# Kernel tuning notes

Hardware: AMD Instinct MI355X
Metric: run time of the kernel (lower is better)

Reference implementation:

```python
import jax, jax.numpy as jnp
import numpy as np

N = 12500      # nodes
E = 200000     # edges (avg degree 16)
IN = 32        # inp_dim
OUT = 32       # out_dim
ATTN = 32      # attn_rel_emb_dim
R = 200        # num_rels
NB = 50        # num_bases


def setup_inputs() -> dict:
    key = jax.random.key(0)
    ks = jax.random.split(key, 10)
    node_feat = jax.random.normal(ks[0], (N, IN), jnp.float32)
    total_edge = jax.random.randint(ks[1], (2, E), 0, N)
    total_target_relation = jax.random.normal(ks[2], (E, ATTN), jnp.float32)
    total_relation_embed = jax.random.normal(ks[3], (E, ATTN), jnp.float32)
    total_relation = jax.random.randint(ks[4], (E,), 0, R)
    # learned parameters (xavier-ish scale)
    weight = jax.random.normal(ks[5], (NB, IN, OUT), jnp.float32) * 0.1
    w_comp = jax.random.normal(ks[6], (R, NB), jnp.float32) * 0.1
    self_loop_weight = jax.random.normal(ks[7], (IN, OUT), jnp.float32) * 0.1
    A_w = jax.random.normal(ks[8], (IN, 2 * IN + 2 * ATTN), jnp.float32) * 0.1
    A_b = jnp.zeros((IN,), jnp.float32)
    B_w = jax.random.normal(ks[9], (1, IN), jnp.float32) * 0.1
    B_b = jnp.zeros((1,), jnp.float32)
    return {
        'node_feat': node_feat,
        'total_target_relation': total_target_relation,
        'total_relation_embed': total_relation_embed,
        'weight': weight,
        'w_comp': w_comp,
        'self_loop_weight': self_loop_weight,
        'A_w': A_w,
        'A_b': A_b,
        'B_w': B_w,
        'B_b': B_b,
        'total_edge': total_edge,
        'total_relation': total_relation,
    }


def reference(node_feat, total_target_relation, total_relation_embed,
              weight, w_comp, self_loop_weight, A_w, A_b, B_w, B_b,
              total_edge, total_relation):
    # basis decomposition: per-relation weight [R, IN, OUT]
    rel_w = jnp.einsum('rb,bio->rio', w_comp, weight)
    src = node_feat[total_edge[0]]            # [E, IN]
    tgt = node_feat[total_edge[1]]            # [E, IN]
    # per-edge relation-specific transform (bmm in torch)
    msg = jnp.einsum('ei,eio->eo', src, rel_w[total_relation])  # [E, OUT]
    curr = tgt @ self_loop_weight             # [E, OUT]
    # attention MLP: sigmoid(B(relu(A(concat))))
    e = jnp.concatenate([src, tgt, total_relation_embed, total_target_relation], axis=1)
    h = jax.nn.relu(e @ A_w.T + A_b)
    a = jax.nn.sigmoid(h @ B_w.T + B_b)       # [E, 1]
    curr = curr + msg * a
    # gnn_spmm(e2n_sp, curr): scatter-add edge messages to target nodes
    out = jax.ops.segment_sum(curr, total_edge[1], num_segments=node_feat.shape[0])
    return out  # [N, OUT]
```

## Files before the change

kernel.cpp:

```cpp
#include <hip/hip_runtime.h>

#define N_NODES 12500
#define N_EDGES 200000
#define DIM 32
#define N_REL 200
#define N_BASES 50

#define OUT_ELEMS   (N_NODES * DIM)
#define ZERO_BLOCKS ((OUT_ELEMS + 1023) / 1024)

#define AWBF_OFF  (N_REL * 1024 * 2)
#define SLWT_OFF  (AWBF_OFF + 32 * 128 * 2)

typedef __attribute__((ext_vector_type(8))) short short8;
typedef __attribute__((ext_vector_type(4))) float f32x4;
typedef __attribute__((ext_vector_type(4))) unsigned short us4;

__device__ __forceinline__ unsigned short f2bf(float x) {
    union { float f; unsigned u; } v; v.f = x;
    unsigned r = (v.u + 0x7FFFu + ((v.u >> 16) & 1u)) >> 16;
    return (unsigned short)r;
}

__device__ __forceinline__ short8 cvt8(float4 a, float4 b) {
    short8 r;
    r[0] = (short)f2bf(a.x); r[1] = (short)f2bf(a.y);
    r[2] = (short)f2bf(a.z); r[3] = (short)f2bf(a.w);
    r[4] = (short)f2bf(b.x); r[5] = (short)f2bf(b.y);
    r[6] = (short)f2bf(b.z); r[7] = (short)f2bf(b.w);
    return r;
}

#define MFMA(A, B, C) __builtin_amdgcn_mfma_f32_16x16x32_bf16(A, B, C, 0, 0, 0)

__global__ __launch_bounds__(256) void prep_kernel(
    const float* __restrict__ weight,
    const float* __restrict__ w_comp,
    const float* __restrict__ Aw,
    const float* __restrict__ slw,
    unsigned short* __restrict__ relw_bf,
    unsigned short* __restrict__ aw_bf,
    unsigned short* __restrict__ slwT_bf,
    float* __restrict__ out)
{
    int b = blockIdx.x, tid = threadIdx.x;
    if (b < N_REL) {
        __shared__ float wc[N_BASES];
        if (tid < N_BASES) wc[tid] = w_comp[b * N_BASES + tid];
        __syncthreads();
        const float* wp = weight + tid * 4;
        float4 acc = make_float4(0.f, 0.f, 0.f, 0.f);
        #pragma unroll 10
        for (int bb = 0; bb < N_BASES; bb++) {
            float4 w = *(const float4*)(wp + bb * 1024);
            float c = wc[bb];
            acc.x = fmaf(c, w.x, acc.x); acc.y = fmaf(c, w.y, acc.y);
            acc.z = fmaf(c, w.z, acc.z); acc.w = fmaf(c, w.w, acc.w);
        }
        us4 o;
        o[0] = f2bf(acc.x); o[1] = f2bf(acc.y);
        o[2] = f2bf(acc.z); o[3] = f2bf(acc.w);
        *(us4*)(relw_bf + b * 1024 + tid * 4) = o;
    } else if (b < N_REL + ZERO_BLOCKS) {
        int base = (b - N_REL) * 1024 + tid * 4;
        if (base + 3 < OUT_ELEMS)
            *(float4*)(out + base) = make_float4(0.f, 0.f, 0.f, 0.f);
        else
            for (int k = 0; k < 4; k++)
                if (base + k < OUT_ELEMS) out[base + k] = 0.f;
    } else {
        for (int x = tid; x < 32 * 128; x += 256) aw_bf[x] = f2bf(Aw[x]);
        for (int x = tid; x < 32 * 32; x += 256) {
            int i = x >> 5, j = x & 31;
            slwT_bf[j * 32 + i] = f2bf(slw[x]);
        }
    }
}

__global__ __launch_bounds__(256) void edge_kernel(
    const float* __restrict__ node_feat,
    const float* __restrict__ ttr,
    const float* __restrict__ tre,
    const float* __restrict__ Ab,
    const float* __restrict__ Bw,
    const float* __restrict__ Bb,
    const int*  __restrict__ edge0,
    const int*  __restrict__ edge1,
    const int*  __restrict__ rel,
    const unsigned short* __restrict__ relw_bf,
    const unsigned short* __restrict__ aw_bf,
    const unsigned short* __restrict__ slwT_bf,
    float* __restrict__ out)
{
    __shared__ float msgL[4 * 16 * 36];

    int tid  = threadIdx.x;
    int wave = tid >> 6;
    int lane = tid & 63;
    int m = lane & 15;
    int q = lane >> 4;
    int base = blockIdx.x * 64 + wave * 16;

    int s_ld = 0, t_ld = 0, r_ld = 0;
    if (lane < 16) {
        int eid = base + lane;
        int s = edge0[eid]; s_ld = s < 0 ? 0 : (s >= N_NODES ? N_NODES - 1 : s);
        int t = edge1[eid]; t_ld = t < 0 ? 0 : (t >= N_NODES ? N_NODES - 1 : t);
        int r = rel[eid];   r_ld = r < 0 ? 0 : (r >= N_REL   ? N_REL   - 1 : r);
    }
    int s_m = __shfl(s_ld, m, 64);
    int t_m = __shfl(t_ld, m, 64);
    int eid_m = base + m;

    const float* sp = node_feat + s_m * DIM + q * 8;
    float4 sv0 = *(const float4*)sp, sv1 = *(const float4*)(sp + 4);
    const float* tp = node_feat + t_m * DIM + q * 8;
    float4 tv0 = *(const float4*)tp, tv1 = *(const float4*)(tp + 4);
    const float* rp = tre + eid_m * DIM + q * 8;
    float4 rv0 = *(const float4*)rp, rv1 = *(const float4*)(rp + 4);
    const float* qp = ttr + eid_m * DIM + q * 8;
    float4 qv0 = *(const float4*)qp, qv1 = *(const float4*)(qp + 4);

    short8 fsrc = cvt8(sv0, sv1);
    short8 ftgt = cvt8(tv0, tv1);
    short8 fre  = cvt8(rv0, rv1);
    short8 ftr  = cvt8(qv0, qv1);

    short8 bA[4][2], bS[2];
    #pragma unroll
    for (int hh = 0; hh < 2; hh++) {
        #pragma unroll
        for (int c = 0; c < 4; c++)
            bA[c][hh] = *(const short8*)(aw_bf + (16 * hh + m) * 128 + 32 * c + 8 * q);
        bS[hh] = *(const short8*)(slwT_bf + (16 * hh + m) * 32 + 8 * q);
    }

    float ab0 = Ab[m], ab1 = Ab[16 + m];
    f32x4 hacc0 = {ab0, ab0, ab0, ab0};
    f32x4 hacc1 = {ab1, ab1, ab1, ab1};
    f32x4 cacc0 = {0.f, 0.f, 0.f, 0.f};
    f32x4 cacc1 = {0.f, 0.f, 0.f, 0.f};

    hacc0 = MFMA(fsrc, bA[0][0], hacc0);  hacc1 = MFMA(fsrc, bA[0][1], hacc1);
    hacc0 = MFMA(ftgt, bA[1][0], hacc0);  hacc1 = MFMA(ftgt, bA[1][1], hacc1);
    hacc0 = MFMA(fre,  bA[2][0], hacc0);  hacc1 = MFMA(fre,  bA[2][1], hacc1);
    hacc0 = MFMA(ftr,  bA[3][0], hacc0);  hacc1 = MFMA(ftr,  bA[3][1], hacc1);
    cacc0 = MFMA(ftgt, bS[0], cacc0);     cacc1 = MFMA(ftgt, bS[1], cacc1);

    int e_loc = lane >> 2;
    int cq    = lane & 3;
    int r_e = __shfl(r_ld, e_loc, 64);
    const unsigned short* rwb = relw_bf + r_e * 1024 + cq * 8;
    float sf[8] = {sv0.x, sv0.y, sv0.z, sv0.w, sv1.x, sv1.y, sv1.z, sv1.w};
    float msg[8] = {0.f, 0.f, 0.f, 0.f, 0.f, 0.f, 0.f, 0.f};
    #pragma unroll
    for (int k = 0; k < 32; k++) {
        float s_k = __shfl(sf[k & 7], e_loc + 16 * (k >> 3), 64);
        union { short8 s; unsigned u[4]; } W;
        W.s = *(const short8*)(rwb + k * 32);
        #pragma unroll
        for (int p = 0; p < 4; p++) {
            float lo = __uint_as_float(W.u[p] << 16);
            float hi = __uint_as_float(W.u[p] & 0xffff0000u);
            msg[2 * p]     = fmaf(s_k, lo, msg[2 * p]);
            msg[2 * p + 1] = fmaf(s_k, hi, msg[2 * p + 1]);
        }
    }

    float* ml = msgL + wave * (16 * 36);
    *(float4*)(ml + e_loc * 36 + cq * 8)     = make_float4(msg[0], msg[1], msg[2], msg[3]);
    *(float4*)(ml + e_loc * 36 + cq * 8 + 4) = make_float4(msg[4], msg[5], msg[6], msg[7]);

    float bw0 = Bw[m], bw1 = Bw[16 + m], Bb0 = Bb[0];
    float av[4];
    #pragma unroll
    for (int v = 0; v < 4; v++) {
        float p = fmaxf(hacc0[v], 0.f) * bw0 + fmaxf(hacc1[v], 0.f) * bw1;
        p += __shfl_xor(p, 1, 16);
        p += __shfl_xor(p, 2, 16);
        p += __shfl_xor(p, 4, 16);
        p += __shfl_xor(p, 8, 16);
        av[v] = 1.f / (1.f + __expf(-(p + Bb0)));
    }
    #pragma unroll
    for (int v = 0; v < 4; v++) {
        int row = 4 * q + v;
        int tv = __shfl(t_ld, row, 64);
        float m0 = ml[row * 36 + m];
        float m1 = ml[row * 36 + 16 + m];
        atomicAdd(&out[tv * DIM + m],      cacc0[v] + m0 * av[v]);
        atomicAdd(&out[tv * DIM + 16 + m], cacc1[v] + m1 * av[v]);
    }
}

extern "C" void kernel_launch(void* const* d_in, const int* in_sizes, int n_in,
                              void* d_out, int out_size, void* d_ws, size_t ws_size,
                              hipStream_t stream) {
    const float* node_feat = (const float*)d_in[0];
    const float* ttr       = (const float*)d_in[1];
    const float* tre       = (const float*)d_in[2];
    const float* weight    = (const float*)d_in[3];
    const float* w_comp    = (const float*)d_in[4];
    const float* slw       = (const float*)d_in[5];
    const float* Aw        = (const float*)d_in[6];
    const float* Ab        = (const float*)d_in[7];
    const float* Bw        = (const float*)d_in[8];
    const float* Bb        = (const float*)d_in[9];
    const int*  total_edge = (const int*)d_in[10];
    const int*  rel        = (const int*)d_in[11];
    const int*  edge0 = total_edge;
    const int*  edge1 = total_edge + N_EDGES;

    unsigned short* relw_bf = (unsigned short*)d_ws;
    unsigned short* aw_bf   = (unsigned short*)((char*)d_ws + AWBF_OFF);
    unsigned short* slwT_bf = (unsigned short*)((char*)d_ws + SLWT_OFF);
    float* out = (float*)d_out;

    prep_kernel<<<N_REL + ZERO_BLOCKS + 1, 256, 0, stream>>>(
        weight, w_comp, Aw, slw, relw_bf, aw_bf, slwT_bf, out);

    edge_kernel<<<N_EDGES / 64, 256, 0, stream>>>(
        node_feat, ttr, tre, Ab, Bw, Bb,
        edge0, edge1, rel, relw_bf, aw_bf, slwT_bf, out);
}
```

Baseline: 152.8 us.

## Counting-sort edges by relation so per-edge weight reads share relation matrices

Adds histogram, serial scan and scatter kernels that build a permutation of edges grouped by relation type, and the edge kernel processes edges in that order. The aim is for the rows of each wave to share the same relation weight matrix, which should improve cache locality for the per-relation weight loads. In exchange it adds three kernel launches, including a single-thread scan. Edge-indexed feature rows (tre/ttr) and the scatter targets are now read and written in scattered rather than contiguous order, which may cost more than the weight locality saves.

```diff
diff --git a/kernel.cpp b/kernel.cpp
--- a/kernel.cpp
+++ b/kernel.cpp
@@ -9,8 +9,15 @@
 #define OUT_ELEMS   (N_NODES * DIM)
 #define ZERO_BLOCKS ((OUT_ELEMS + 1023) / 1024)
 
-#define AWBF_OFF  (N_REL * 1024 * 2)
-#define SLWT_OFF  (AWBF_OFF + 32 * 128 * 2)
+#define EDGES_PER_HBLOCK 1024
+#define HIST_BLOCKS ((N_EDGES + EDGES_PER_HBLOCK - 1) / EDGES_PER_HBLOCK)
+
+#define AWBF_OFF  409600
+#define SLWT_OFF  417792
+#define BINS_OFF  419840
+#define CURS_OFF  420864
+#define PERM_OFF  421888
+#define WS_NEEDED (PERM_OFF + N_EDGES * 4)
 
 typedef __attribute__((ext_vector_type(8))) short short8;
 typedef __attribute__((ext_vector_type(4))) float f32x4;
@@ -29,6 +36,10 @@
     r[4] = (short)f2bf(b.x); r[5] = (short)f2bf(b.y);
     r[6] = (short)f2bf(b.z); r[7] = (short)f2bf(b.w);
     return r;
+}
+
+__device__ __forceinline__ int clampi(int x, int hi) {
+    return x < 0 ? 0 : (x >= hi ? hi - 1 : x);
 }
 
 #define MFMA(A, B, C) __builtin_amdgcn_mfma_f32_16x16x32_bf16(A, B, C, 0, 0, 0)
@@ -41,6 +52,7 @@
     unsigned short* __restrict__ relw_bf,
     unsigned short* __restrict__ aw_bf,
     unsigned short* __restrict__ slwT_bf,
+    int* __restrict__ bins,
     float* __restrict__ out)
 {
     int b = blockIdx.x, tid = threadIdx.x;
@@ -74,7 +86,64 @@
             int i = x >> 5, j = x & 31;
             slwT_bf[j * 32 + i] = f2bf(slw[x]);
         }
-    }
+        if (tid < N_REL) bins[tid] = 0;
+    }
+}
+
+__global__ __launch_bounds__(256) void hist_kernel(
+    const int* __restrict__ rel, int* __restrict__ bins)
+{
+    __shared__ int lb[N_REL];
+    int tid = threadIdx.x;
+    if (tid < N_REL) lb[tid] = 0;
+    __syncthreads();
+    int base = blockIdx.x * EDGES_PER_HBLOCK + tid;
+    #pragma unroll
+    for (int k = 0; k < 4; k++) {
+        int e = base + k * 256;
+        if (e < N_EDGES) atomicAdd(&lb[clampi(rel[e], N_REL)], 1);
+    }
+    __syncthreads();
+    if (tid < N_REL && lb[tid] > 0) atomicAdd(&bins[tid], lb[tid]);
+}
+
+__global__ __launch_bounds__(64) void scan_kernel(
+    const int* __restrict__ bins, int* __restrict__ cursors)
+{
+    if (threadIdx.x == 0) {
+        int run = 0;
+        for (int r = 0; r < N_REL; r++) { cursors[r] = run; run += bins[r]; }
+    }
+}
+
+__global__ __launch_bounds__(256) void scatter_kernel(
+    const int* __restrict__ rel, int* __restrict__ cursors,
+    int* __restrict__ perm)
+{
+    __shared__ int lb[N_REL];
+    int tid = threadIdx.x;
+    if (tid < N_REL) lb[tid] = 0;
+    __syncthreads();
+    int base = blockIdx.x * EDGES_PER_HBLOCK + tid;
+    int myr[4], myrank[4];
+    #pragma unroll
+    for (int k = 0; k < 4; k++) {
+        int e = base + k * 256;
+        myr[k] = -1;
+        if (e < N_EDGES) {
+            myr[k] = clampi(rel[e], N_REL);
+            myrank[k] = atomicAdd(&lb[myr[k]], 1);
+        }
+    }
+    __syncthreads();
+    if (tid < N_REL) {
+        int c = lb[tid];
+        lb[tid] = c > 0 ? atomicAdd(&cursors[tid], c) : 0;
+    }
+    __syncthreads();
+    #pragma unroll
+    for (int k = 0; k < 4; k++)
+        if (myr[k] >= 0) perm[lb[myr[k]] + myrank[k]] = base + k * 256;
 }
 
 __global__ __launch_bounds__(256) void edge_kernel(
@@ -87,6 +156,7 @@
     const int*  __restrict__ edge0,
     const int*  __restrict__ edge1,
     const int*  __restrict__ rel,
+    const int*  __restrict__ perm,
     const unsigned short* __restrict__ relw_bf,
     const unsigned short* __restrict__ aw_bf,
     const unsigned short* __restrict__ slwT_bf,
@@ -101,16 +171,18 @@
     int q = lane >> 4;
     int base = blockIdx.x * 64 + wave * 16;
 
-    int s_ld = 0, t_ld = 0, r_ld = 0;
+    int s_ld = 0, t_ld = 0, r_ld = 0, e_ld = 0;
     if (lane < 16) {
-        int eid = base + lane;
-        int s = edge0[eid]; s_ld = s < 0 ? 0 : (s >= N_NODES ? N_NODES - 1 : s);
-        int t = edge1[eid]; t_ld = t < 0 ? 0 : (t >= N_NODES ? N_NODES - 1 : t);
-        int r = rel[eid];   r_ld = r < 0 ? 0 : (r >= N_REL   ? N_REL   - 1 : r);
-    }
-    int s_m = __shfl(s_ld, m, 64);
-    int t_m = __shfl(t_ld, m, 64);
-    int eid_m = base + m;
+        int eid = perm ? perm[base + lane] : (base + lane);
+        eid = clampi(eid, N_EDGES);
+        e_ld = eid;
+        s_ld = clampi(edge0[eid], N_NODES);
+        t_ld = clampi(edge1[eid], N_NODES);
+        r_ld = clampi(rel[eid],   N_REL);
+    }
+    int s_m   = __shfl(s_ld, m, 64);
+    int t_m   = __shfl(t_ld, m, 64);
+    int eid_m = __shfl(e_ld, m, 64);
 
     const float* sp = node_feat + s_m * DIM + q * 8;
     float4 sv0 = *(const float4*)sp, sv1 = *(const float4*)(sp + 4);
@@ -214,12 +286,24 @@
     unsigned short* relw_bf = (unsigned short*)d_ws;
     unsigned short* aw_bf   = (unsigned short*)((char*)d_ws + AWBF_OFF);
     unsigned short* slwT_bf = (unsigned short*)((char*)d_ws + SLWT_OFF);
+    int* bins    = (int*)((char*)d_ws + BINS_OFF);
+    int* cursors = (int*)((char*)d_ws + CURS_OFF);
+    int* perm    = (int*)((char*)d_ws + PERM_OFF);
     float* out = (float*)d_out;
 
+    bool use_sort = ws_size >= (size_t)WS_NEEDED;
+
     prep_kernel<<<N_REL + ZERO_BLOCKS + 1, 256, 0, stream>>>(
-        weight, w_comp, Aw, slw, relw_bf, aw_bf, slwT_bf, out);
+        weight, w_comp, Aw, slw, relw_bf, aw_bf, slwT_bf, bins, out);
+
+    if (use_sort) {
+        hist_kernel<<<HIST_BLOCKS, 256, 0, stream>>>(rel, bins);
+        scan_kernel<<<1, 64, 0, stream>>>(bins, cursors);
+        scatter_kernel<<<HIST_BLOCKS, 256, 0, stream>>>(rel, cursors, perm);
+    }
 
     edge_kernel<<<N_EDGES / 64, 256, 0, stream>>>(
         node_feat, ttr, tre, Ab, Bw, Bb,
-        edge0, edge1, rel, relw_bf, aw_bf, slwT_bf, out);
-}
+        edge0, edge1, rel, use_sort ? perm : (const int*)nullptr,
+        relw_bf, aw_bf, slwT_bf, out);
+}
```

Result: slower. 165.9 us (+8.6%).
